# Kernel optimization log

Measured on AMD Instinct MI355X. Metric: run time of the kernel, lower is better.

Reference implementation:

```python
import jax, jax.numpy as jnp
import numpy as np

KERNEL_MUL = 2.0
KERNEL_NUM = 5
SIZE = 128  # hardcoded slice size in the original forward


def setup_inputs() -> dict:
    key = jax.random.key(0)
    k1, k2 = jax.random.split(key)
    B, D, S = 64, 4096, 128
    source = jax.random.normal(k1, (B, D, S), dtype=jnp.float32)
    target = jax.random.normal(k2, (B, D, S), dtype=jnp.float32)
    return {"source": source, "target": target}


def _mmd_rbf(source, target):
    # source/target: [B, D, S] with S == SIZE
    B, D, S = source.shape
    # per-sample: permute to [S, D] and concat -> total: [B, 2S, D]
    x = jnp.concatenate(
        [jnp.transpose(source, (0, 2, 1)), jnp.transpose(target, (0, 2, 1))], axis=1
    )
    n = 2 * S
    sq = jnp.sum(x * x, axis=-1)  # [B, 2S]
    # pairwise squared L2 via Gram matrix (avoids [2S,2S,D] expansion)
    gram = jnp.einsum("bnd,bmd->bnm", x, x)  # [B, 2S, 2S]
    L2 = sq[:, :, None] + sq[:, None, :] - 2.0 * gram  # [B, 2S, 2S]
    # bandwidth from detached distances (torch uses L2_distance.data)
    bw = jax.lax.stop_gradient(jnp.sum(L2, axis=(1, 2))) / (n * n - n)  # [B]
    bw = bw / (KERNEL_MUL ** (KERNEL_NUM // 2))
    scales = KERNEL_MUL ** jnp.arange(KERNEL_NUM, dtype=jnp.float32)  # [K]
    bws = bw[:, None, None, None] * scales[None, :, None, None]  # [B, K, 1, 1]
    kernels = jnp.sum(jnp.exp(-L2[:, None, :, :] / bws), axis=1)  # [B, 2S, 2S]
    K = jnp.mean(kernels, axis=0)  # sum over batch / B -> [2S, 2S]
    loss = (
        jnp.mean(K[:SIZE, :SIZE])
        + jnp.mean(K[SIZE:, SIZE:])
        - jnp.mean(K[:SIZE, SIZE:])
        - jnp.mean(K[SIZE:, :SIZE])
    )
    return loss


def reference(source, target):
    return _mmd_rbf(source, target)
```

## Files before the change

kernel.cpp:

```cpp
#include <hip/hip_runtime.h>

#define B_  64
#define D_  4096
#define S_  128
#define N_  256
#define KC_ 4
#define KPB (D_ / KC_)
#define BK  64
#define NCH (KPB / BK)
#define RS  72
#define LDSBUF (N_ * RS)
#define TILE_ (N_ * N_)

using short8   = __attribute__((ext_vector_type(8)))  short;
using floatx16 = __attribute__((ext_vector_type(16))) float;

__device__ __forceinline__ unsigned int pk2(float lo, float hi) {
  unsigned int r;
  asm("v_cvt_pk_bf16_f32 %0, %1, %2" : "=v"(r) : "v"(lo), "v"(hi));
  return r;
}

__device__ __forceinline__ int swz(int n, int g) {
  return n * RS + ((g ^ (n & 3) ^ ((n >> 3) & 3)) << 3);
}

__global__ __launch_bounds__(512, 4) void k_gram(
    const float* __restrict__ src, const float* __restrict__ tgt,
    float* __restrict__ partial, float* __restrict__ tot,
    float* __restrict__ sq) {
  __shared__ unsigned short lds[2 * LDSBUF];
  __shared__ float red[8];
  const int bx  = blockIdx.x;
  const int kc  = bx >> 1;
  const int rh  = bx & 1;
  const int b   = blockIdx.y;
  const int tid = threadIdx.x;
  const int l   = tid & 63;
  const int w   = tid >> 6;
  const int tr  = w >> 2;
  const int tc  = w & 3;

  const int n_s = tid & 255;
  const int g   = tid >> 8;
  const float* colbase = (n_s < S_)
      ? (src + (size_t)b * D_ * S_ + n_s)
      : (tgt + (size_t)b * D_ * S_ + (n_s - S_));
  const float* pA = colbase + (size_t)kc * KPB * S_;

  float ld[16];
  floatx16 acc[2][2];
  #pragma unroll
  for (int i = 0; i < 2; i++)
    #pragma unroll
    for (int j = 0; j < 2; j++)
      #pragma unroll
      for (int r = 0; r < 16; r++) acc[i][j][r] = 0.f;

  const int lm   = l & 31;
  const int lk   = l >> 5;
  const int ar   = rh * 128 + tr * 64 + lm;
  const int bcol = tc * 64 + lm;

  #define LOADH(ch, gb)                                                \
    do {                                                               \
      const float* q = pA + (size_t)(ch) * BK * S_;                    \
      _Pragma("unroll")                                                \
      for (int j = 0; j < 8; j++) {                                    \
        ld[j]     = q[(size_t)(((gb)) * 8 + j) * S_];                  \
        ld[8 + j] = q[(size_t)(((gb) + 2) * 8 + j) * S_];              \
      }                                                                \
    } while (0)

  #define WRITEH(buf, gb)                                              \
    do {                                                               \
      uint4 wa, wb;                                                    \
      wa.x = pk2(ld[0],  ld[1]);                                       \
      wa.y = pk2(ld[2],  ld[3]);                                       \
      wa.z = pk2(ld[4],  ld[5]);                                       \
      wa.w = pk2(ld[6],  ld[7]);                                       \
      wb.x = pk2(ld[8],  ld[9]);                                       \
      wb.y = pk2(ld[10], ld[11]);                                      \
      wb.z = pk2(ld[12], ld[13]);                                      \
      wb.w = pk2(ld[14], ld[15]);                                      \
      const int base_ = (buf) * LDSBUF;                                \
      *(uint4*)&lds[base_ + swz(n_s, (gb))]     = wa;                  \
      *(uint4*)&lds[base_ + swz(n_s, (gb) + 2)] = wb;                  \
    } while (0)

  #define MFMA2(buf, k0)                                               \
    do {                                                               \
      const unsigned short* L = &lds[(buf) * LDSBUF];                  \
      _Pragma("unroll")                                                \
      for (int ks = (k0); ks < (k0) + 2; ks++) {                       \
        const int gg = ks * 2 + lk;                                    \
        short8 a0 = *(const short8*)&L[swz(ar,        gg)];            \
        short8 a1 = *(const short8*)&L[swz(ar + 32,   gg)];            \
        short8 b0 = *(const short8*)&L[swz(bcol,      gg)];            \
        short8 b1 = *(const short8*)&L[swz(bcol + 32, gg)];            \
        acc[0][0] = __builtin_amdgcn_mfma_f32_32x32x16_bf16(a0, b0, acc[0][0], 0, 0, 0); \
        acc[0][1] = __builtin_amdgcn_mfma_f32_32x32x16_bf16(a0, b1, acc[0][1], 0, 0, 0); \
        acc[1][0] = __builtin_amdgcn_mfma_f32_32x32x16_bf16(a1, b0, acc[1][0], 0, 0, 0); \
        acc[1][1] = __builtin_amdgcn_mfma_f32_32x32x16_bf16(a1, b1, acc[1][1], 0, 0, 0); \
      }                                                                \
    } while (0)

  LOADH(0, g);
  WRITEH(0, g);
  LOADH(0, g + 4);
  WRITEH(0, g + 4);
  __syncthreads();
  for (int ch = 0; ch < NCH - 1; ch++) {
    LOADH(ch + 1, g);
    MFMA2(ch & 1, 0);
    WRITEH((ch + 1) & 1, g);
    LOADH(ch + 1, g + 4);
    MFMA2(ch & 1, 2);
    WRITEH((ch + 1) & 1, g + 4);
    __syncthreads();
  }
  MFMA2((NCH - 1) & 1, 0);
  MFMA2((NCH - 1) & 1, 2);

  float* gb = partial + ((size_t)kc * B_ + b) * TILE_;
  #pragma unroll
  for (int i = 0; i < 2; i++)
    #pragma unroll
    for (int j = 0; j < 2; j++)
      #pragma unroll
      for (int r = 0; r < 16; r++) {
        const int row = (r & 3) + 8 * (r >> 2) + 4 * lk;
        const int nr  = rh * 128 + tr * 64 + i * 32 + row;
        const int nc  = tc * 64 + j * 32 + (l & 31);
        gb[nr * N_ + nc] = acc[i][j][r];
      }

  float s = 0.f;
  #pragma unroll
  for (int i = 0; i < 2; i++)
    #pragma unroll
    for (int j = 0; j < 2; j++)
      #pragma unroll
      for (int r = 0; r < 16; r++) s += acc[i][j][r];
  for (int off = 32; off; off >>= 1) s += __shfl_down(s, off);
  if (l == 0) red[w] = s;
  __syncthreads();
  if (tid == 0) {
    float T = red[0] + red[1] + red[2] + red[3]
            + red[4] + red[5] + red[6] + red[7];
    atomicAdd(&tot[b], T);
  }

  if ((rh * 2 + tr) == tc && lk == ((l >> 2) & 1)) {
    const int c = l & 31;
    const int r = (c >> 3) * 4 + (c & 3);
    #pragma unroll
    for (int i = 0; i < 2; i++)
      atomicAdd(&sq[b * N_ + tc * 64 + i * 32 + c], acc[i][i][r]);
  }
  #undef LOADH
  #undef WRITEH
  #undef MFMA2
}

__global__ __launch_bounds__(512, 4) void k_exp(
    const float* __restrict__ partial, const float* __restrict__ tot,
    const float* __restrict__ sq, float* __restrict__ out) {
  __shared__ float sqs[N_];
  __shared__ float red[8];
  __shared__ float bws;
  const int rc = blockIdx.x;
  const int b  = blockIdx.y;
  const int t  = threadIdx.x;
  const int cg = t & 63;
  const int rg = t >> 6;

  if (t < N_) sqs[t] = sq[b * N_ + t];
  __syncthreads();
  if (t < N_) {
    float v = sqs[t];
    for (int off = 32; off; off >>= 1) v += __shfl_down(v, off);
    if ((t & 63) == 0) red[t >> 6] = v;
  }
  __syncthreads();
  if (t == 0) {
    float ssq = red[0] + red[1] + red[2] + red[3];
    float SL2 = 2.f * (float)N_ * ssq - 2.f * tot[b];
    bws = SL2 / (float)(N_ * N_ - N_) * 0.25f;
  }
  __syncthreads();

  const float bwv = bws;
  float nb[5];
  #pragma unroll
  for (int k = 0; k < 5; k++)
    nb[k] = -1.4426950408889634f / (bwv * (float)(1 << k));

  const int c4 = cg * 4;
  const float4 sqc = *(const float4*)&sqs[c4];
  const float sgn = ((rc < 4) == (cg < 32)) ? 1.f : -1.f;
  const float* p0 = partial + (size_t)b * TILE_;

  float accv = 0.f;
  #pragma unroll
  for (int r = 0; r < 4; r++) {
    const int row = rc * 32 + rg * 4 + r;
    const float4 g0 = *(const float4*)&p0[row * N_ + c4];
    const float4 g1 = *(const float4*)&p0[(size_t)1 * B_ * TILE_ + row * N_ + c4];
    const float4 g2 = *(const float4*)&p0[(size_t)2 * B_ * TILE_ + row * N_ + c4];
    const float4 g3 = *(const float4*)&p0[(size_t)3 * B_ * TILE_ + row * N_ + c4];
    const float sr = sqs[row];
    float4 L2;
    L2.x = sr + sqc.x - 2.f * (g0.x + g1.x + g2.x + g3.x);
    L2.y = sr + sqc.y - 2.f * (g0.y + g1.y + g2.y + g3.y);
    L2.z = sr + sqc.z - 2.f * (g0.z + g1.z + g2.z + g3.z);
    L2.w = sr + sqc.w - 2.f * (g0.w + g1.w + g2.w + g3.w);
    #pragma unroll
    for (int k = 0; k < 5; k++) {
      accv += exp2f(L2.x * nb[k]) + exp2f(L2.y * nb[k])
            + exp2f(L2.z * nb[k]) + exp2f(L2.w * nb[k]);
    }
  }
  accv *= sgn;
  for (int off = 32; off; off >>= 1) accv += __shfl_down(accv, off);
  __syncthreads();
  if ((t & 63) == 0) red[t >> 6] = accv;
  __syncthreads();
  if (t == 0) {
    float s2 = red[0] + red[1] + red[2] + red[3]
             + red[4] + red[5] + red[6] + red[7];
    atomicAdd(out, s2 * (1.0f / (64.f * 16384.f)));
  }
}

extern "C" void kernel_launch(void* const* d_in, const int* in_sizes, int n_in,
                              void* d_out, int out_size, void* d_ws, size_t ws_size,
                              hipStream_t stream) {
  const float* src = (const float*)d_in[0];
  const float* tgt = (const float*)d_in[1];
  const size_t partial_bytes = (size_t)KC_ * B_ * TILE_ * sizeof(float);
  float* partial = (float*)d_ws;
  float* tot     = (float*)((char*)d_ws + partial_bytes);
  float* sq      = tot + B_;
  hipMemsetAsync(tot, 0, (B_ + B_ * N_) * sizeof(float), stream);
  hipMemsetAsync(d_out, 0, sizeof(float), stream);
  k_gram<<<dim3(KC_ * 2, B_), 512, 0, stream>>>(src, tgt, partial, tot, sq);
  k_exp<<<dim3(8, B_), 512, 0, stream>>>(partial, tot, sq, (float*)d_out);
}
```

Measured before the change: 309.4 us.

## Compute full 256x256 Gram tile per block instead of splitting rows across two blocks

Each block now computes the whole 256x256 Gram tile for its K-chunk, with each wave owning a 64x128 subtile (2x4 MFMA accumulators). Previously two blocks each loaded the entire K-chunk into LDS but used only half the rows. This halves redundant global loads and bf16 conversion per output. Both global load halves are now issued before the MFMAs for deeper prefetch, and the LDS swizzle is simplified. In exchange, register pressure roughly doubles (launch bounds drop to 2 blocks per CU) and the grid halves to 256 blocks.

```diff
diff --git a/kernel.cpp b/kernel.cpp
--- a/kernel.cpp
+++ b/kernel.cpp
@@ -22,24 +22,22 @@
 }
 
 __device__ __forceinline__ int swz(int n, int g) {
-  return n * RS + ((g ^ (n & 3) ^ ((n >> 3) & 3)) << 3);
-}
-
-__global__ __launch_bounds__(512, 4) void k_gram(
+  return n * RS + ((g ^ ((n >> 3) & 3)) << 3);
+}
+
+__global__ __launch_bounds__(512, 2) void k_gram(
     const float* __restrict__ src, const float* __restrict__ tgt,
     float* __restrict__ partial, float* __restrict__ tot,
     float* __restrict__ sq) {
   __shared__ unsigned short lds[2 * LDSBUF];
   __shared__ float red[8];
-  const int bx  = blockIdx.x;
-  const int kc  = bx >> 1;
-  const int rh  = bx & 1;
+  const int kc  = blockIdx.x;
   const int b   = blockIdx.y;
   const int tid = threadIdx.x;
   const int l   = tid & 63;
   const int w   = tid >> 6;
-  const int tr  = w >> 2;
-  const int tc  = w & 3;
+  const int wr  = w >> 1;
+  const int wc  = w & 1;
 
   const int n_s = tid & 255;
   const int g   = tid >> 8;
@@ -48,47 +46,47 @@
       : (tgt + (size_t)b * D_ * S_ + (n_s - S_));
   const float* pA = colbase + (size_t)kc * KPB * S_;
 
-  float ld[16];
-  floatx16 acc[2][2];
+  float ld[16], ld2[16];
+  floatx16 acc[2][4];
   #pragma unroll
   for (int i = 0; i < 2; i++)
     #pragma unroll
-    for (int j = 0; j < 2; j++)
+    for (int j = 0; j < 4; j++)
       #pragma unroll
       for (int r = 0; r < 16; r++) acc[i][j][r] = 0.f;
 
   const int lm   = l & 31;
   const int lk   = l >> 5;
-  const int ar   = rh * 128 + tr * 64 + lm;
-  const int bcol = tc * 64 + lm;
-
-  #define LOADH(ch, gb)                                                \
+  const int ar   = wr * 64 + lm;
+  const int bcol = wc * 128 + lm;
+
+  #define LOADH(arr, ch, gb)                                           \
     do {                                                               \
       const float* q = pA + (size_t)(ch) * BK * S_;                    \
       _Pragma("unroll")                                                \
       for (int j = 0; j < 8; j++) {                                    \
-        ld[j]     = q[(size_t)(((gb)) * 8 + j) * S_];                  \
-        ld[8 + j] = q[(size_t)(((gb) + 2) * 8 + j) * S_];              \
+        arr[j]     = q[(size_t)(((gb)) * 8 + j) * S_];                 \
+        arr[8 + j] = q[(size_t)(((gb) + 2) * 8 + j) * S_];             \
       }                                                                \
     } while (0)
 
-  #define WRITEH(buf, gb)                                              \
+  #define WRITEH(arr, buf, gb)                                         \
     do {                                                               \
       uint4 wa, wb;                                                    \
-      wa.x = pk2(ld[0],  ld[1]);                                       \
-      wa.y = pk2(ld[2],  ld[3]);                                       \
-      wa.z = pk2(ld[4],  ld[5]);                                       \
-      wa.w = pk2(ld[6],  ld[7]);                                       \
-      wb.x = pk2(ld[8],  ld[9]);                                       \
-      wb.y = pk2(ld[10], ld[11]);                                      \
-      wb.z = pk2(ld[12], ld[13]);                                      \
-      wb.w = pk2(ld[14], ld[15]);                                      \
+      wa.x = pk2(arr[0],  arr[1]);                                     \
+      wa.y = pk2(arr[2],  arr[3]);                                     \
+      wa.z = pk2(arr[4],  arr[5]);                                     \
+      wa.w = pk2(arr[6],  arr[7]);                                     \
+      wb.x = pk2(arr[8],  arr[9]);                                     \
+      wb.y = pk2(arr[10], arr[11]);                                    \
+      wb.z = pk2(arr[12], arr[13]);                                    \
+      wb.w = pk2(arr[14], arr[15]);                                    \
       const int base_ = (buf) * LDSBUF;                                \
       *(uint4*)&lds[base_ + swz(n_s, (gb))]     = wa;                  \
       *(uint4*)&lds[base_ + swz(n_s, (gb) + 2)] = wb;                  \
     } while (0)
 
-  #define MFMA2(buf, k0)                                               \
+  #define MFMA4(buf, k0)                                               \
     do {                                                               \
       const unsigned short* L = &lds[(buf) * LDSBUF];                  \
       _Pragma("unroll")                                                \
@@ -98,40 +96,46 @@
         short8 a1 = *(const short8*)&L[swz(ar + 32,   gg)];            \
         short8 b0 = *(const short8*)&L[swz(bcol,      gg)];            \
         short8 b1 = *(const short8*)&L[swz(bcol + 32, gg)];            \
+        short8 b2 = *(const short8*)&L[swz(bcol + 64, gg)];            \
+        short8 b3 = *(const short8*)&L[swz(bcol + 96, gg)];            \
         acc[0][0] = __builtin_amdgcn_mfma_f32_32x32x16_bf16(a0, b0, acc[0][0], 0, 0, 0); \
         acc[0][1] = __builtin_amdgcn_mfma_f32_32x32x16_bf16(a0, b1, acc[0][1], 0, 0, 0); \
+        acc[0][2] = __builtin_amdgcn_mfma_f32_32x32x16_bf16(a0, b2, acc[0][2], 0, 0, 0); \
+        acc[0][3] = __builtin_amdgcn_mfma_f32_32x32x16_bf16(a0, b3, acc[0][3], 0, 0, 0); \
         acc[1][0] = __builtin_amdgcn_mfma_f32_32x32x16_bf16(a1, b0, acc[1][0], 0, 0, 0); \
         acc[1][1] = __builtin_amdgcn_mfma_f32_32x32x16_bf16(a1, b1, acc[1][1], 0, 0, 0); \
+        acc[1][2] = __builtin_amdgcn_mfma_f32_32x32x16_bf16(a1, b2, acc[1][2], 0, 0, 0); \
+        acc[1][3] = __builtin_amdgcn_mfma_f32_32x32x16_bf16(a1, b3, acc[1][3], 0, 0, 0); \
       }                                                                \
     } while (0)
 
-  LOADH(0, g);
-  WRITEH(0, g);
-  LOADH(0, g + 4);
-  WRITEH(0, g + 4);
+  LOADH(ld,  0, g);
+  LOADH(ld2, 0, g + 4);
+  WRITEH(ld,  0, g);
+  WRITEH(ld2, 0, g + 4);
   __syncthreads();
   for (int ch = 0; ch < NCH - 1; ch++) {
-    LOADH(ch + 1, g);
-    MFMA2(ch & 1, 0);
-    WRITEH((ch + 1) & 1, g);
-    LOADH(ch + 1, g + 4);
-    MFMA2(ch & 1, 2);
-    WRITEH((ch + 1) & 1, g + 4);
+    LOADH(ld,  ch + 1, g);
+    LOADH(ld2, ch + 1, g + 4);
+    MFMA4(ch & 1, 0);
+    WRITEH(ld, (ch + 1) & 1, g);
+    MFMA4(ch & 1, 2);
+    WRITEH(ld2, (ch + 1) & 1, g + 4);
     __syncthreads();
   }
-  MFMA2((NCH - 1) & 1, 0);
-  MFMA2((NCH - 1) & 1, 2);
+  MFMA4((NCH - 1) & 1, 0);
+  MFMA4((NCH - 1) & 1, 2);
 
   float* gb = partial + ((size_t)kc * B_ + b) * TILE_;
   #pragma unroll
   for (int i = 0; i < 2; i++)
     #pragma unroll
-    for (int j = 0; j < 2; j++)
+    for (int j = 0; j < 4; j++)
       #pragma unroll
       for (int r = 0; r < 16; r++) {
         const int row = (r & 3) + 8 * (r >> 2) + 4 * lk;
-        const int nr  = rh * 128 + tr * 64 + i * 32 + row;
-        const int nc  = tc * 64 + j * 32 + (l & 31);
+        const int nr  = wr * 64 + i * 32 + row;
+        const int nc  = wc * 128 + j * 32 + (l & 31);
         gb[nr * N_ + nc] = acc[i][j][r];
       }
 
@@ -139,7 +143,7 @@
   #pragma unroll
   for (int i = 0; i < 2; i++)
     #pragma unroll
-    for (int j = 0; j < 2; j++)
+    for (int j = 0; j < 4; j++)
       #pragma unroll
       for (int r = 0; r < 16; r++) s += acc[i][j][r];
   for (int off = 32; off; off >>= 1) s += __shfl_down(s, off);
@@ -151,16 +155,17 @@
     atomicAdd(&tot[b], T);
   }
 
-  if ((rh * 2 + tr) == tc && lk == ((l >> 2) & 1)) {
+  if (wc == (wr >> 1) && lk == ((l >> 2) & 1)) {
     const int c = l & 31;
     const int r = (c >> 3) * 4 + (c & 3);
+    const int basej = (wr & 1) * 2;
     #pragma unroll
     for (int i = 0; i < 2; i++)
-      atomicAdd(&sq[b * N_ + tc * 64 + i * 32 + c], acc[i][i][r]);
+      atomicAdd(&sq[b * N_ + wr * 64 + i * 32 + c], acc[i][basej + i][r]);
   }
   #undef LOADH
   #undef WRITEH
-  #undef MFMA2
+  #undef MFMA4
 }
 
 __global__ __launch_bounds__(512, 4) void k_exp(
@@ -244,6 +249,6 @@
   float* sq      = tot + B_;
   hipMemsetAsync(tot, 0, (B_ + B_ * N_) * sizeof(float), stream);
   hipMemsetAsync(d_out, 0, sizeof(float), stream);
-  k_gram<<<dim3(KC_ * 2, B_), 512, 0, stream>>>(src, tgt, partial, tot, sq);
+  k_gram<<<dim3(KC_, B_), 512, 0, stream>>>(src, tgt, partial, tot, sq);
   k_exp<<<dim3(8, B_), 512, 0, stream>>>(partial, tot, sq, (float*)d_out);
 }
```

After: 421.5 us. +36.2%, slower.

## Merge row-half blocks into 1024-thread blocks computing full Gram tile

Applied to the files above, without the earlier changes.

Each block now runs 16 waves and computes the full 256x256 Gram tile for its K-chunk, instead of two 512-thread blocks each computing one row half. Every operand chunk is therefore loaded from global memory and converted once rather than twice. The pipeline now prefetches the global loads two chunks ahead across the MFMA phases, and the LDS swizzle is simplified to match the new write pattern. In exchange the grid halves to 256 blocks, and larger blocks with LDS double-buffering may lower occupancy or load balance across CUs.

```diff
diff --git a/kernel.cpp b/kernel.cpp
--- a/kernel.cpp
+++ b/kernel.cpp
@@ -22,24 +22,22 @@
 }
 
 __device__ __forceinline__ int swz(int n, int g) {
-  return n * RS + ((g ^ (n & 3) ^ ((n >> 3) & 3)) << 3);
-}
-
-__global__ __launch_bounds__(512, 4) void k_gram(
+  return n * RS + ((g ^ ((n >> 3) & 3)) << 3);
+}
+
+__global__ __launch_bounds__(1024, 4) void k_gram(
     const float* __restrict__ src, const float* __restrict__ tgt,
     float* __restrict__ partial, float* __restrict__ tot,
     float* __restrict__ sq) {
   __shared__ unsigned short lds[2 * LDSBUF];
-  __shared__ float red[8];
-  const int bx  = blockIdx.x;
-  const int kc  = bx >> 1;
-  const int rh  = bx & 1;
+  __shared__ float red[16];
+  const int kc  = blockIdx.x;
   const int b   = blockIdx.y;
   const int tid = threadIdx.x;
   const int l   = tid & 63;
   const int w   = tid >> 6;
-  const int tr  = w >> 2;
-  const int tc  = w & 3;
+  const int wr  = w >> 2;
+  const int wc  = w & 3;
 
   const int n_s = tid & 255;
   const int g   = tid >> 8;
@@ -59,20 +57,20 @@
 
   const int lm   = l & 31;
   const int lk   = l >> 5;
-  const int ar   = rh * 128 + tr * 64 + lm;
-  const int bcol = tc * 64 + lm;
-
-  #define LOADH(ch, gb)                                                \
+  const int ar   = wr * 64 + lm;
+  const int bcol = wc * 64 + lm;
+
+  #define LOADH(ch)                                                    \
     do {                                                               \
       const float* q = pA + (size_t)(ch) * BK * S_;                    \
       _Pragma("unroll")                                                \
       for (int j = 0; j < 8; j++) {                                    \
-        ld[j]     = q[(size_t)(((gb)) * 8 + j) * S_];                  \
-        ld[8 + j] = q[(size_t)(((gb) + 2) * 8 + j) * S_];              \
+        ld[j]     = q[(size_t)(g * 8 + j) * S_];                       \
+        ld[8 + j] = q[(size_t)((g + 4) * 8 + j) * S_];                 \
       }                                                                \
     } while (0)
 
-  #define WRITEH(buf, gb)                                              \
+  #define WRITEH(buf)                                                  \
     do {                                                               \
       uint4 wa, wb;                                                    \
       wa.x = pk2(ld[0],  ld[1]);                                       \
@@ -84,11 +82,11 @@
       wb.z = pk2(ld[12], ld[13]);                                      \
       wb.w = pk2(ld[14], ld[15]);                                      \
       const int base_ = (buf) * LDSBUF;                                \
-      *(uint4*)&lds[base_ + swz(n_s, (gb))]     = wa;                  \
-      *(uint4*)&lds[base_ + swz(n_s, (gb) + 2)] = wb;                  \
+      *(uint4*)&lds[base_ + swz(n_s, g)]     = wa;                     \
+      *(uint4*)&lds[base_ + swz(n_s, g + 4)] = wb;                     \
     } while (0)
 
-  #define MFMA2(buf, k0)                                               \
+  #define MFMAH(buf, k0)                                               \
     do {                                                               \
       const unsigned short* L = &lds[(buf) * LDSBUF];                  \
       _Pragma("unroll")                                                \
@@ -105,22 +103,19 @@
       }                                                                \
     } while (0)
 
-  LOADH(0, g);
-  WRITEH(0, g);
-  LOADH(0, g + 4);
-  WRITEH(0, g + 4);
+  LOADH(0);
+  WRITEH(0);
+  LOADH(1);
   __syncthreads();
   for (int ch = 0; ch < NCH - 1; ch++) {
-    LOADH(ch + 1, g);
-    MFMA2(ch & 1, 0);
-    WRITEH((ch + 1) & 1, g);
-    LOADH(ch + 1, g + 4);
-    MFMA2(ch & 1, 2);
-    WRITEH((ch + 1) & 1, g + 4);
+    MFMAH(ch & 1, 0);
+    WRITEH((ch + 1) & 1);
+    if (ch + 2 < NCH) LOADH(ch + 2);
+    MFMAH(ch & 1, 2);
     __syncthreads();
   }
-  MFMA2((NCH - 1) & 1, 0);
-  MFMA2((NCH - 1) & 1, 2);
+  MFMAH((NCH - 1) & 1, 0);
+  MFMAH((NCH - 1) & 1, 2);
 
   float* gb = partial + ((size_t)kc * B_ + b) * TILE_;
   #pragma unroll
@@ -130,8 +125,8 @@
       #pragma unroll
       for (int r = 0; r < 16; r++) {
         const int row = (r & 3) + 8 * (r >> 2) + 4 * lk;
-        const int nr  = rh * 128 + tr * 64 + i * 32 + row;
-        const int nc  = tc * 64 + j * 32 + (l & 31);
+        const int nr  = wr * 64 + i * 32 + row;
+        const int nc  = wc * 64 + j * 32 + (l & 31);
         gb[nr * N_ + nc] = acc[i][j][r];
       }
 
@@ -146,21 +141,22 @@
   if (l == 0) red[w] = s;
   __syncthreads();
   if (tid == 0) {
-    float T = red[0] + red[1] + red[2] + red[3]
-            + red[4] + red[5] + red[6] + red[7];
+    float T = 0.f;
+    #pragma unroll
+    for (int i = 0; i < 16; i++) T += red[i];
     atomicAdd(&tot[b], T);
   }
 
-  if ((rh * 2 + tr) == tc && lk == ((l >> 2) & 1)) {
+  if (wr == wc && lk == ((l >> 2) & 1)) {
     const int c = l & 31;
     const int r = (c >> 3) * 4 + (c & 3);
     #pragma unroll
     for (int i = 0; i < 2; i++)
-      atomicAdd(&sq[b * N_ + tc * 64 + i * 32 + c], acc[i][i][r]);
+      atomicAdd(&sq[b * N_ + wr * 64 + i * 32 + c], acc[i][i][r]);
   }
   #undef LOADH
   #undef WRITEH
-  #undef MFMA2
+  #undef MFMAH
 }
 
 __global__ __launch_bounds__(512, 4) void k_exp(
@@ -244,6 +240,6 @@
   float* sq      = tot + B_;
   hipMemsetAsync(tot, 0, (B_ + B_ * N_) * sizeof(float), stream);
   hipMemsetAsync(d_out, 0, sizeof(float), stream);
-  k_gram<<<dim3(KC_ * 2, B_), 512, 0, stream>>>(src, tgt, partial, tot, sq);
+  k_gram<<<dim3(KC_, B_), 1024, 0, stream>>>(src, tgt, partial, tot, sq);
   k_exp<<<dim3(8, B_), 512, 0, stream>>>(partial, tot, sq, (float*)d_out);
 }
```

After: 309.9 us. No clear change (+0.2%).
